# Optimization experiments

Hardware: AMD Instinct MI355X
Metric: run time of the kernel (lower is better)

The kernel has to match this reference:

```python
import jax, jax.numpy as jnp
import numpy as np

PSIZE = 3
PSTRIDE = 3
N = PSIZE * PSTRIDE   # 9 attention tokens
P = PSIZE ** 2        # 9 pixels per token


def setup_inputs() -> dict:
    key = jax.random.key(0)
    k1, k2, k3, k4, k5 = jax.random.split(key, 5)
    B, H, W, C = 8192, 9, 9, 256
    hidden = C // 2
    x = jax.random.normal(k1, (B, H, W, C), dtype=jnp.float32)
    W_fc = jax.random.normal(k2, (hidden, C), dtype=jnp.float32) * (C ** -0.5)
    b_fc = jax.random.normal(k3, (hidden,), dtype=jnp.float32) * 0.01
    block_idx = jax.random.randint(k4, (B,), 0, 1024, dtype=jnp.int32)
    match_vec = jax.random.randint(k5, (1024, 1), 0, 2, dtype=jnp.int32)
    return {"x": x, "W_fc": W_fc, "b_fc": b_fc, "block_idx": block_idx, "match_vec": match_vec}


def reference(x, W_fc, b_fc, block_idx, match_vec):
    B, H, Wd, C = x.shape
    hidden = W_fc.shape[0]
    scale = (hidden * P) ** -0.5

    # [B, pstride, psize, pstride, psize, C] -> patch-major [B, ps, ps, p, p, C]
    xv = x.reshape(B, PSTRIDE, PSIZE, PSTRIDE, PSIZE, C).transpose(0, 1, 3, 2, 4, 5)
    x_fc = xv.reshape(B, N, P, C)

    # linear projection C -> hidden, then flatten pixels: q [B, N, P*hidden]
    q = (jnp.einsum('bnpc,hc->bnph', x_fc, W_fc) + b_fc).reshape(B, N, P * hidden)

    attn = jnp.einsum('bnd,bmd->bnm', q, q) * scale  # [B, N, N]

    # additive mask: -100 on diagonal, zeroed out entirely for matched samples
    base = jnp.where(jnp.eye(N, dtype=bool), jnp.float32(-100.0), jnp.float32(0.0))
    cur_match = match_vec[block_idx].squeeze(-1)  # [B]
    mask = jnp.where(cur_match[:, None, None] == 1, jnp.float32(0.0), base[None])

    attn = jax.nn.softmax(attn + mask, axis=-1)

    v = xv.reshape(B, N, P * C)
    out = attn @ v  # [B, N, P*C]

    out = out.reshape(B, PSTRIDE, PSTRIDE, PSIZE, PSIZE, C)
    out = out.transpose(0, 1, 3, 2, 4, 5).reshape(B, H, Wd, C)
    return out
```

## Files before the change

kernel.cpp:

```cpp
#include <hip/hip_runtime.h>

typedef short short8 __attribute__((ext_vector_type(8)));
typedef float floatx16 __attribute__((ext_vector_type(16)));
typedef float floatx4 __attribute__((ext_vector_type(4)));

#define ROWS 81
#define CDIM 256
#define XT   0
#define QT   41472
#define SC   66048
#define AB   70144
#define TOT  70656

#define SWX(r) ((((r) & 15) << 4) ^ (((r) & 8) << 3))

__device__ __forceinline__ unsigned short f2bf(float f) {
    union { float f; unsigned int u; } v; v.f = f;
    return (unsigned short)((v.u + 0x7FFFu + ((v.u >> 16) & 1u)) >> 16);
}

__device__ __forceinline__ unsigned int cvtpk(float lo, float hi) {
    unsigned int r;
    asm("v_cvt_pk_bf16_f32 %0, %1, %2" : "=v"(r) : "v"(lo), "v"(hi));
    return r;
}

__global__ void wconv_kernel(const float* __restrict__ W,
                             unsigned short* __restrict__ Wb, int n) {
    int i = blockIdx.x * 256 + threadIdx.x;
    if (i < n) Wb[i] = f2bf(W[i]);
}

__device__ __forceinline__ void stage_store(char* smem, int k, float4 a0, float4 a1) {
    int gr = k >> 5;
    int c0 = (k & 31) * 8;
    int hh = gr / 9, ww = gr - hh * 9;
    int p = (hh % 3) * 3 + (ww % 3);
    int m = (hh / 3) * 3 + (ww / 3);
    int r = p * 9 + m;
    uint4 v;
    v.x = cvtpk(a0.x, a0.y);
    v.y = cvtpk(a0.z, a0.w);
    v.z = cvtpk(a1.x, a1.y);
    v.w = cvtpk(a1.z, a1.w);
    *(uint4*)(smem + XT + r * 512 + ((c0 * 2) ^ SWX(r))) = v;
}

__global__ __launch_bounds__(512, 4)
void attn_kernel(const float* __restrict__ x,
                 const unsigned short* __restrict__ Wb,
                 const float* __restrict__ b_fc,
                 const int* __restrict__ block_idx,
                 const int* __restrict__ match_vec,
                 float* __restrict__ out)
{
    __shared__ __align__(16) char smem[TOT];
    const int b     = blockIdx.x;
    const int t     = threadIdx.x;
    const int lane  = t & 63;
    const int wave  = t >> 6;
    const int l15   = lane & 15;
    const int kg    = lane >> 4;
    const int l31   = lane & 31;
    const int khalf = lane >> 5;

    if (b < 512 && (((b ^ (b >> 8)) & 1) != 0)) {
        __builtin_amdgcn_s_sleep(100);
        __builtin_amdgcn_s_sleep(100);
    }

    int cm = 0;
    if (t < 9) cm = match_vec[block_idx[b]];

    const int rh = (wave & 1) * 48;
    const int hg = (wave >> 1) * 32;

    short8 wfrag[2][8];
#pragma unroll
    for (int s2 = 0; s2 < 2; ++s2) {
        const unsigned short* wr = Wb + (hg + s2 * 16 + l15) * CDIM + kg * 8;
#pragma unroll
        for (int ks = 0; ks < 8; ++ks)
            wfrag[s2][ks] = *(const short8*)(wr + ks * 32);
    }
    float bias2[2];
    bias2[0] = b_fc[hg + l15];
    bias2[1] = b_fc[hg + 16 + l15];

    {
        const float* xb = x + (size_t)b * (ROWS * CDIM);
        for (int k = t; k < ROWS * 32; k += 512) {
            float4 a0 = *(const float4*)(xb + k * 8);
            float4 a1 = *(const float4*)(xb + k * 8 + 4);
            stage_store(smem, k, a0, a1);
        }
    }
    __syncthreads();

    {
        floatx4 acc[3][2];
#pragma unroll
        for (int ii = 0; ii < 3; ++ii)
#pragma unroll
            for (int s2 = 0; s2 < 2; ++s2)
#pragma unroll
                for (int j = 0; j < 4; ++j) acc[ii][s2][j] = 0.f;
#pragma unroll
        for (int ks = 0; ks < 8; ++ks) {
            int cb = ks * 64 + kg * 16;
#pragma unroll
            for (int tile = 0; tile < 3; ++tile) {
                int r = rh + tile * 16 + l15;
                short8 a = *(const short8*)(smem + XT + r * 512 + (cb ^ SWX(r)));
                acc[tile][0] = __builtin_amdgcn_mfma_f32_16x16x32_bf16(a, wfrag[0][ks], acc[tile][0], 0, 0, 0);
                acc[tile][1] = __builtin_amdgcn_mfma_f32_16x16x32_bf16(a, wfrag[1][ks], acc[tile][1], 0, 0, 0);
            }
        }
#pragma unroll
        for (int tile = 0; tile < 3; ++tile)
#pragma unroll
            for (int s2 = 0; s2 < 2; ++s2) {
                int h2 = (hg + s2 * 16 + l15) * 2;
#pragma unroll
                for (int reg = 0; reg < 4; ++reg) {
                    int r = rh + tile * 16 + kg * 4 + reg;
                    *(unsigned short*)(smem + QT + r * 256 + (h2 ^ ((r & 15) << 4))) =
                        f2bf(acc[tile][s2][reg] + bias2[s2]);
                }
            }
    }
    __syncthreads();

    if (wave < 4) {
        floatx4 g;
#pragma unroll
        for (int ii = 0; ii < 4; ++ii) g[ii] = 0.f;
        int nc = (l15 < 9) ? l15 : 8;
#pragma unroll
        for (int s = 0; s < 9; ++s) {
            int ks = wave + s * 4;
            int kk = ks * 32 + kg * 8;
            int p  = kk >> 7;
            int h0 = (kk & 127) * 2;
            int row = p * 9 + nc;
            short8 f = *(const short8*)(smem + QT + row * 256 + (h0 ^ ((row & 15) << 4)));
            g = __builtin_amdgcn_mfma_f32_16x16x32_bf16(f, f, g, 0, 0, 0);
        }
        float* sc = (float*)(smem + SC + wave * 1024);
#pragma unroll
        for (int reg = 0; reg < 4; ++reg)
            sc[(kg * 4 + reg) * 16 + l15] = g[reg];
    }
    __syncthreads();

    if (t < 9) {
        const float scale = 0.029462782549439483f;
        const float* sc0 = (const float*)(smem + SC);
        const float* sc1 = (const float*)(smem + SC + 1024);
        const float* sc2 = (const float*)(smem + SC + 2048);
        const float* sc3 = (const float*)(smem + SC + 3072);
        float s[9];
        float mx = -1e30f;
#pragma unroll
        for (int m = 0; m < 9; ++m) {
            int o = t * 16 + m;
            float v = (sc0[o] + sc1[o] + sc2[o] + sc3[o]) * scale;
            if (m == t && cm != 1) v -= 100.f;
            s[m] = v;
            mx = fmaxf(mx, v);
        }
        float sum = 0.f;
#pragma unroll
        for (int m = 0; m < 9; ++m) { s[m] = __expf(s[m] - mx); sum += s[m]; }
        float inv = 1.f / sum;
        unsigned short* ab = (unsigned short*)(smem + AB) + t * 16;
#pragma unroll
        for (int m = 0; m < 9; ++m) ab[m] = f2bf(s[m] * inv);
#pragma unroll
        for (int m = 9; m < 16; ++m) ab[m] = 0;
    }
    __syncthreads();

    {
        const int n  = l31;
        const int nm = (n < 9) ? n : 0;
        short8 bf = *(const short8*)(smem + AB + nm * 32 + khalf * 16);
        floatx16 zero16;
#pragma unroll
        for (int ii = 0; ii < 16; ++ii) zero16[ii] = 0.f;
        float* ob = out + (size_t)b * (ROWS * CDIM);
        int hh = 0, ww = 0;
        if (n < 9) { hh = (n / 3) * 3; ww = (n % 3) * 3; }
#pragma unroll
        for (int tt = 0; tt < 9; ++tt) {
            int tile = wave * 9 + tt;
            int p = tile >> 3;
            int c = (tile & 7) * 32 + l31;
            short8 af;
#pragma unroll
            for (int j = 0; j < 8; ++j) {
                int mm = khalf * 8 + j; if (mm > 8) mm = 8;
                int row = p * 9 + mm;
                af[j] = *(const short*)(smem + XT + row * 512 + ((c * 2) ^ SWX(row)));
            }
            floatx16 dacc = __builtin_amdgcn_mfma_f32_32x32x16_bf16(af, bf, zero16, 0, 0, 0);
            if (n < 9) {
#pragma unroll
                for (int q2 = 0; q2 < 4; ++q2) {
                    int c0 = (tile & 7) * 32 + q2 * 8 + khalf * 4;
                    int gr = (hh + p / 3) * 9 + (ww + p % 3);
                    *(float4*)(ob + gr * CDIM + c0) =
                        make_float4(dacc[q2 * 4 + 0], dacc[q2 * 4 + 1],
                                    dacc[q2 * 4 + 2], dacc[q2 * 4 + 3]);
                }
            }
        }
    }
}

extern "C" void kernel_launch(void* const* d_in, const int* in_sizes, int n_in,
                              void* d_out, int out_size, void* d_ws, size_t ws_size,
                              hipStream_t stream) {
    const float* x    = (const float*)d_in[0];
    const float* W    = (const float*)d_in[1];
    const float* bfc  = (const float*)d_in[2];
    const int*   bidx = (const int*)d_in[3];
    const int*   mvec = (const int*)d_in[4];
    float* outp = (float*)d_out;
    unsigned short* Wb = (unsigned short*)d_ws;

    int nW = in_sizes[1];
    wconv_kernel<<<(nW + 255) / 256, 256, 0, stream>>>(W, Wb, nW);

    int B = in_sizes[0] / (ROWS * CDIM);
    attn_kernel<<<B, 512, 0, stream>>>(x, Wb, bfc, bidx, mvec, outp);
}
```

Baseline: 378.3 us.

## Use persistent 1024-thread blocks with async LDS prefetch of next sample

Replaces one-block-per-sample launch with 256 persistent blocks of 1024 threads, each looping over samples. While computing the current sample, it prefetches the next sample's raw fp32 tile into LDS via global_load_lds. The attn@V product now uses scalar FMAs on register-held bf16 values instead of MFMA with gathered short loads, and the artificial s_sleep staggering is removed. The 150KB LDS footprint limits occupancy to one block per CU, and a 256-block grid may underfill the device.

```diff
diff --git a/kernel.cpp b/kernel.cpp
--- a/kernel.cpp
+++ b/kernel.cpp
@@ -1,18 +1,25 @@
 #include <hip/hip_runtime.h>
 
 typedef short short8 __attribute__((ext_vector_type(8)));
-typedef float floatx16 __attribute__((ext_vector_type(16)));
 typedef float floatx4 __attribute__((ext_vector_type(4)));
 
 #define ROWS 81
 #define CDIM 256
-#define XT   0
-#define QT   41472
-#define SC   66048
-#define AB   70144
-#define TOT  70656
+#define NTHR 1024
+#define RAW  0
+#define XT   82944
+#define QT   124416
+#define SC   148992
+#define AB   153088
+#define TOT  153600
 
 #define SWX(r) ((((r) & 15) << 4) ^ (((r) & 8) << 3))
+
+#define BAR_LGKM() asm volatile("s_waitcnt lgkmcnt(0)\n\ts_barrier" ::: "memory")
+
+#define GLOAD16(g, l) __builtin_amdgcn_global_load_lds( \
+    (const __attribute__((address_space(1))) unsigned int*)(g), \
+    (__attribute__((address_space(3))) unsigned int*)(l), 16, 0, 0)
 
 __device__ __forceinline__ unsigned short f2bf(float f) {
     union { float f; unsigned int u; } v; v.f = f;
@@ -25,194 +32,224 @@
     return r;
 }
 
+__device__ __forceinline__ float bflo(unsigned int u) { return __uint_as_float(u << 16); }
+__device__ __forceinline__ float bfhi(unsigned int u) { return __uint_as_float(u & 0xffff0000u); }
+
 __global__ void wconv_kernel(const float* __restrict__ W,
                              unsigned short* __restrict__ Wb, int n) {
     int i = blockIdx.x * 256 + threadIdx.x;
     if (i < n) Wb[i] = f2bf(W[i]);
 }
 
-__device__ __forceinline__ void stage_store(char* smem, int k, float4 a0, float4 a1) {
-    int gr = k >> 5;
-    int c0 = (k & 31) * 8;
-    int hh = gr / 9, ww = gr - hh * 9;
-    int p = (hh % 3) * 3 + (ww % 3);
-    int m = (hh / 3) * 3 + (ww / 3);
-    int r = p * 9 + m;
-    uint4 v;
-    v.x = cvtpk(a0.x, a0.y);
-    v.y = cvtpk(a0.z, a0.w);
-    v.z = cvtpk(a1.x, a1.y);
-    v.w = cvtpk(a1.z, a1.w);
-    *(uint4*)(smem + XT + r * 512 + ((c0 * 2) ^ SWX(r))) = v;
-}
-
-__global__ __launch_bounds__(512, 4)
-void attn_kernel(const float* __restrict__ x,
-                 const unsigned short* __restrict__ Wb,
-                 const float* __restrict__ b_fc,
-                 const int* __restrict__ block_idx,
-                 const int* __restrict__ match_vec,
-                 float* __restrict__ out)
+__global__ void __launch_bounds__(NTHR, 4)
+attn_kernel(const float* __restrict__ x,
+            const unsigned short* __restrict__ Wb,
+            const float* __restrict__ b_fc,
+            const int* __restrict__ block_idx,
+            const int* __restrict__ match_vec,
+            float* __restrict__ out,
+            int B, int nIter)
 {
     __shared__ __align__(16) char smem[TOT];
-    const int b     = blockIdx.x;
     const int t     = threadIdx.x;
     const int lane  = t & 63;
     const int wave  = t >> 6;
     const int l15   = lane & 15;
     const int kg    = lane >> 4;
-    const int l31   = lane & 31;
-    const int khalf = lane >> 5;
-
-    if (b < 512 && (((b ^ (b >> 8)) & 1) != 0)) {
-        __builtin_amdgcn_s_sleep(100);
-        __builtin_amdgcn_s_sleep(100);
-    }
-
-    int cm = 0;
-    if (t < 9) cm = match_vec[block_idx[b]];
-
-    const int rh = (wave & 1) * 48;
-    const int hg = (wave >> 1) * 32;
+    const int base  = blockIdx.x * nIter;
+    if (base >= B) return;
+
+    const int rg = wave >> 2;
+    const int hg = wave & 3;
 
     short8 wfrag[2][8];
 #pragma unroll
     for (int s2 = 0; s2 < 2; ++s2) {
-        const unsigned short* wr = Wb + (hg + s2 * 16 + l15) * CDIM + kg * 8;
+        const unsigned short* wr = Wb + (hg * 32 + s2 * 16 + l15) * CDIM + kg * 8;
 #pragma unroll
         for (int ks = 0; ks < 8; ++ks)
             wfrag[s2][ks] = *(const short8*)(wr + ks * 32);
     }
     float bias2[2];
-    bias2[0] = b_fc[hg + l15];
-    bias2[1] = b_fc[hg + 16 + l15];
+    bias2[0] = b_fc[hg * 32 + l15];
+    bias2[1] = b_fc[hg * 32 + 16 + l15];
+
+    int rawoff[6], xtoff[6];
+#pragma unroll
+    for (int j = 0; j < 6; ++j) {
+        int u = t + 1024 * j;
+        rawoff[j] = RAW + u * 16;
+        int gr = u >> 6;
+        int c0 = (u & 63) * 4;
+        int hh = gr / 9, ww = gr - hh * 9;
+        int p  = (hh % 3) * 3 + (ww % 3);
+        int m  = (hh / 3) * 3 + (ww / 3);
+        int r  = p * 9 + m;
+        xtoff[j] = XT + r * 512 + ((c0 * 2) ^ SWX(r));
+    }
+    const int p_ = (t < 576) ? (t >> 6) : 0;
+    const int c_ = (lane) * 4;
+    int groff[9];
+#pragma unroll
+    for (int k = 0; k < 9; ++k) {
+        int hh = (k / 3) * 3 + p_ / 3;
+        int ww = (k % 3) * 3 + p_ % 3;
+        groff[k] = (hh * 9 + ww) * CDIM + c_;
+    }
 
     {
-        const float* xb = x + (size_t)b * (ROWS * CDIM);
-        for (int k = t; k < ROWS * 32; k += 512) {
-            float4 a0 = *(const float4*)(xb + k * 8);
-            float4 a1 = *(const float4*)(xb + k * 8 + 4);
-            stage_store(smem, k, a0, a1);
-        }
-    }
-    __syncthreads();
-
-    {
-        floatx4 acc[3][2];
-#pragma unroll
-        for (int ii = 0; ii < 3; ++ii)
-#pragma unroll
-            for (int s2 = 0; s2 < 2; ++s2)
-#pragma unroll
-                for (int j = 0; j < 4; ++j) acc[ii][s2][j] = 0.f;
-#pragma unroll
-        for (int ks = 0; ks < 8; ++ks) {
-            int cb = ks * 64 + kg * 16;
-#pragma unroll
-            for (int tile = 0; tile < 3; ++tile) {
-                int r = rh + tile * 16 + l15;
-                short8 a = *(const short8*)(smem + XT + r * 512 + (cb ^ SWX(r)));
-                acc[tile][0] = __builtin_amdgcn_mfma_f32_16x16x32_bf16(a, wfrag[0][ks], acc[tile][0], 0, 0, 0);
-                acc[tile][1] = __builtin_amdgcn_mfma_f32_16x16x32_bf16(a, wfrag[1][ks], acc[tile][1], 0, 0, 0);
-            }
-        }
-#pragma unroll
-        for (int tile = 0; tile < 3; ++tile)
-#pragma unroll
-            for (int s2 = 0; s2 < 2; ++s2) {
-                int h2 = (hg + s2 * 16 + l15) * 2;
-#pragma unroll
-                for (int reg = 0; reg < 4; ++reg) {
-                    int r = rh + tile * 16 + kg * 4 + reg;
-                    *(unsigned short*)(smem + QT + r * 256 + (h2 ^ ((r & 15) << 4))) =
-                        f2bf(acc[tile][s2][reg] + bias2[s2]);
-                }
-            }
-    }
-    __syncthreads();
-
-    if (wave < 4) {
-        floatx4 g;
-#pragma unroll
-        for (int ii = 0; ii < 4; ++ii) g[ii] = 0.f;
-        int nc = (l15 < 9) ? l15 : 8;
-#pragma unroll
-        for (int s = 0; s < 9; ++s) {
-            int ks = wave + s * 4;
-            int kk = ks * 32 + kg * 8;
-            int p  = kk >> 7;
-            int h0 = (kk & 127) * 2;
-            int row = p * 9 + nc;
-            short8 f = *(const short8*)(smem + QT + row * 256 + (h0 ^ ((row & 15) << 4)));
-            g = __builtin_amdgcn_mfma_f32_16x16x32_bf16(f, f, g, 0, 0, 0);
-        }
-        float* sc = (float*)(smem + SC + wave * 1024);
-#pragma unroll
-        for (int reg = 0; reg < 4; ++reg)
-            sc[(kg * 4 + reg) * 16 + l15] = g[reg];
-    }
-    __syncthreads();
-
-    if (t < 9) {
-        const float scale = 0.029462782549439483f;
-        const float* sc0 = (const float*)(smem + SC);
-        const float* sc1 = (const float*)(smem + SC + 1024);
-        const float* sc2 = (const float*)(smem + SC + 2048);
-        const float* sc3 = (const float*)(smem + SC + 3072);
-        float s[9];
-        float mx = -1e30f;
-#pragma unroll
-        for (int m = 0; m < 9; ++m) {
-            int o = t * 16 + m;
-            float v = (sc0[o] + sc1[o] + sc2[o] + sc3[o]) * scale;
-            if (m == t && cm != 1) v -= 100.f;
-            s[m] = v;
-            mx = fmaxf(mx, v);
-        }
-        float sum = 0.f;
-#pragma unroll
-        for (int m = 0; m < 9; ++m) { s[m] = __expf(s[m] - mx); sum += s[m]; }
-        float inv = 1.f / sum;
-        unsigned short* ab = (unsigned short*)(smem + AB) + t * 16;
-#pragma unroll
-        for (int m = 0; m < 9; ++m) ab[m] = f2bf(s[m] * inv);
-#pragma unroll
-        for (int m = 9; m < 16; ++m) ab[m] = 0;
-    }
-    __syncthreads();
-
-    {
-        const int n  = l31;
-        const int nm = (n < 9) ? n : 0;
-        short8 bf = *(const short8*)(smem + AB + nm * 32 + khalf * 16);
-        floatx16 zero16;
-#pragma unroll
-        for (int ii = 0; ii < 16; ++ii) zero16[ii] = 0.f;
-        float* ob = out + (size_t)b * (ROWS * CDIM);
-        int hh = 0, ww = 0;
-        if (n < 9) { hh = (n / 3) * 3; ww = (n % 3) * 3; }
-#pragma unroll
-        for (int tt = 0; tt < 9; ++tt) {
-            int tile = wave * 9 + tt;
-            int p = tile >> 3;
-            int c = (tile & 7) * 32 + l31;
-            short8 af;
-#pragma unroll
-            for (int j = 0; j < 8; ++j) {
-                int mm = khalf * 8 + j; if (mm > 8) mm = 8;
-                int row = p * 9 + mm;
-                af[j] = *(const short*)(smem + XT + row * 512 + ((c * 2) ^ SWX(row)));
-            }
-            floatx16 dacc = __builtin_amdgcn_mfma_f32_32x32x16_bf16(af, bf, zero16, 0, 0, 0);
-            if (n < 9) {
-#pragma unroll
-                for (int q2 = 0; q2 < 4; ++q2) {
-                    int c0 = (tile & 7) * 32 + q2 * 8 + khalf * 4;
-                    int gr = (hh + p / 3) * 9 + (ww + p % 3);
-                    *(float4*)(ob + gr * CDIM + c0) =
-                        make_float4(dacc[q2 * 4 + 0], dacc[q2 * 4 + 1],
-                                    dacc[q2 * 4 + 2], dacc[q2 * 4 + 3]);
-                }
+        const float* xb = x + (size_t)base * (ROWS * CDIM);
+#pragma unroll
+        for (int j = 0; j < 6; ++j)
+            if (j < 5 || t < 64) GLOAD16(xb + (t + 1024 * j) * 4, smem + rawoff[j]);
+    }
+
+    for (int it = 0; it < nIter && base + it < B; ++it) {
+        const int b = base + it;
+        const bool hasNext = (it + 1 < nIter) && (b + 1 < B);
+
+        int cm = 0;
+        if (t < 9) cm = match_vec[block_idx[b]];
+
+        __syncthreads();
+
+#pragma unroll
+        for (int j = 0; j < 6; ++j) {
+            if (j < 5 || t < 64) {
+                float4 a = *(const float4*)(smem + rawoff[j]);
+                uint2 w;
+                w.x = cvtpk(a.x, a.y);
+                w.y = cvtpk(a.z, a.w);
+                *(uint2*)(smem + xtoff[j]) = w;
+            }
+        }
+        unsigned v0[9], v1[9];
+        if (t < 576) {
+#pragma unroll
+            for (int m = 0; m < 9; ++m) {
+                float4 q = *(const float4*)(smem + RAW + groff[m] * 4);
+                v0[m] = cvtpk(q.x, q.y);
+                v1[m] = cvtpk(q.z, q.w);
+            }
+        }
+        __syncthreads();
+
+        if (hasNext) {
+            const float* xn = x + (size_t)(b + 1) * (ROWS * CDIM);
+#pragma unroll
+            for (int j = 0; j < 6; ++j)
+                if (j < 5 || t < 64) GLOAD16(xn + (t + 1024 * j) * 4, smem + rawoff[j]);
+        }
+
+        {
+            floatx4 acc[2][2];
+#pragma unroll
+            for (int ti = 0; ti < 2; ++ti)
+#pragma unroll
+                for (int s2 = 0; s2 < 2; ++s2)
+#pragma unroll
+                    for (int j = 0; j < 4; ++j) acc[ti][s2][j] = 0.f;
+#pragma unroll
+            for (int ks = 0; ks < 8; ++ks) {
+                int cb = ks * 64 + kg * 16;
+                {
+                    int r = rg * 24 + l15;
+                    short8 a = *(const short8*)(smem + XT + r * 512 + (cb ^ SWX(r)));
+                    acc[0][0] = __builtin_amdgcn_mfma_f32_16x16x32_bf16(a, wfrag[0][ks], acc[0][0], 0, 0, 0);
+                    acc[0][1] = __builtin_amdgcn_mfma_f32_16x16x32_bf16(a, wfrag[1][ks], acc[0][1], 0, 0, 0);
+                }
+                if (rg < 3) {
+                    int r = rg * 24 + 16 + l15;
+                    short8 a = *(const short8*)(smem + XT + r * 512 + (cb ^ SWX(r)));
+                    acc[1][0] = __builtin_amdgcn_mfma_f32_16x16x32_bf16(a, wfrag[0][ks], acc[1][0], 0, 0, 0);
+                    acc[1][1] = __builtin_amdgcn_mfma_f32_16x16x32_bf16(a, wfrag[1][ks], acc[1][1], 0, 0, 0);
+                }
+            }
+#pragma unroll
+            for (int ti = 0; ti < 2; ++ti) {
+                if (ti == 1 && rg == 3) continue;
+#pragma unroll
+                for (int s2 = 0; s2 < 2; ++s2) {
+                    int h2 = (hg * 32 + s2 * 16 + l15) * 2;
+#pragma unroll
+                    for (int reg = 0; reg < 4; ++reg) {
+                        int r = rg * 24 + ti * 16 + kg * 4 + reg;
+                        *(unsigned short*)(smem + QT + r * 256 + (h2 ^ ((r & 15) << 4))) =
+                            f2bf(acc[ti][s2][reg] + bias2[s2]);
+                    }
+                }
+            }
+        }
+        BAR_LGKM();
+
+        if (wave < 4) {
+            floatx4 g;
+#pragma unroll
+            for (int ii = 0; ii < 4; ++ii) g[ii] = 0.f;
+            int nc = (l15 < 9) ? l15 : 8;
+#pragma unroll
+            for (int s = 0; s < 9; ++s) {
+                int ks = wave + s * 4;
+                int kk = ks * 32 + kg * 8;
+                int p  = kk >> 7;
+                int h0 = (kk & 127) * 2;
+                int row = p * 9 + nc;
+                short8 f = *(const short8*)(smem + QT + row * 256 + (h0 ^ ((row & 15) << 4)));
+                g = __builtin_amdgcn_mfma_f32_16x16x32_bf16(f, f, g, 0, 0, 0);
+            }
+            float* sc = (float*)(smem + SC + wave * 1024);
+#pragma unroll
+            for (int reg = 0; reg < 4; ++reg)
+                sc[(kg * 4 + reg) * 16 + l15] = g[reg];
+        }
+        BAR_LGKM();
+
+        if (t < 9) {
+            const float scale = 0.029462782549439483f;
+            const float* sc0 = (const float*)(smem + SC);
+            const float* sc1 = (const float*)(smem + SC + 1024);
+            const float* sc2 = (const float*)(smem + SC + 2048);
+            const float* sc3 = (const float*)(smem + SC + 3072);
+            float s[9];
+            float mx = -1e30f;
+#pragma unroll
+            for (int m = 0; m < 9; ++m) {
+                int o = t * 16 + m;
+                float v = (sc0[o] + sc1[o] + sc2[o] + sc3[o]) * scale;
+                if (m == t && cm != 1) v -= 100.f;
+                s[m] = v;
+                mx = fmaxf(mx, v);
+            }
+            float sum = 0.f;
+#pragma unroll
+            for (int m = 0; m < 9; ++m) { s[m] = __expf(s[m] - mx); sum += s[m]; }
+            float inv = 1.f / sum;
+            float* ab = (float*)(smem + AB) + t * 12;
+#pragma unroll
+            for (int m = 0; m < 9; ++m) ab[m] = s[m] * inv;
+        }
+        BAR_LGKM();
+
+        if (t < 576) {
+            float* ob = out + (size_t)b * (ROWS * CDIM);
+#pragma unroll
+            for (int n = 0; n < 9; ++n) {
+                const float* abr = (const float*)(smem + AB) + n * 12;
+                float4 a03 = *(const float4*)(abr);
+                float4 a47 = *(const float4*)(abr + 4);
+                float  a8  = abr[8];
+                float o0 = 0.f, o1 = 0.f, o2 = 0.f, o3 = 0.f;
+#pragma unroll
+                for (int m = 0; m < 9; ++m) {
+                    float am = (m < 4) ? ((m == 0) ? a03.x : (m == 1) ? a03.y : (m == 2) ? a03.z : a03.w)
+                             : (m < 8) ? ((m == 4) ? a47.x : (m == 5) ? a47.y : (m == 6) ? a47.z : a47.w)
+                             : a8;
+                    o0 += am * bflo(v0[m]);
+                    o1 += am * bfhi(v0[m]);
+                    o2 += am * bflo(v1[m]);
+                    o3 += am * bfhi(v1[m]);
+                }
+                *(float4*)(ob + groff[n]) = make_float4(o0, o1, o2, o3);
             }
         }
     }
@@ -233,5 +270,7 @@
     wconv_kernel<<<(nW + 255) / 256, 256, 0, stream>>>(W, Wb, nW);
 
     int B = in_sizes[0] / (ROWS * CDIM);
-    attn_kernel<<<B, 512, 0, stream>>>(x, Wb, bfc, bidx, mvec, outp);
-}
+    int grid = (B < 256) ? B : 256;
+    int nIter = (B + grid - 1) / grid;
+    attn_kernel<<<grid, NTHR, 0, stream>>>(x, Wb, bfc, bidx, mvec, outp, B, nIter);
+}
```

Result: slower. 1.064 ms (+181.2%).
